# Kernel optimization log

Hardware: AMD Instinct MI355X
Metric: run time of the kernel (lower is better)

The kernel has to match this reference:

```python
import jax, jax.numpy as jnp
import numpy as np


def setup_inputs() -> dict:
    key = jax.random.key(0)
    k1, k2, k3 = jax.random.split(key, 3)
    N, C, Nf, W, H = 8, 256, 16, 28, 28
    l = jax.random.normal(k1, (N, C, Nf, W, H), dtype=jnp.float32)
    g = jax.random.normal(k2, (N, C, 1, 1, 1), dtype=jnp.float32)
    # 1x1x1 Conv3d(in=C, out=1, bias=False) weight collapses to a length-C vector
    w = jax.random.normal(k3, (C,), dtype=jnp.float32) * (1.0 / np.sqrt(C))
    return {"l": l, "g": g, "w": w}


def reference(l, g, w):
    # l: [N,C,Nf,W,H], g broadcastable to l, w: [C]
    N, C, Nf, W, H = l.shape
    # compatibility score: channel dot-product (1x1x1 conv, out_channels=1)
    c = jnp.einsum('ncfwh,c->nfwh', l + g, w)                      # [N,Nf,W,H]
    # softmax over the spatial dims (W*H) per frame, normalize_attn=True
    a = jax.nn.softmax(c.reshape(N, Nf, W * H), axis=-1)           # [N,Nf,WH]
    a = a.reshape(N, Nf, W, H)
    # attention-weighted spatial sum pooling -> [N,C,Nf]
    g_out = jnp.einsum('nfwh,ncfwh->ncf', a, l)
    # module returns raw compatibility map (pre-softmax) squeezed, and pooled g
    return (c, g_out)
```

## Files before the change

kernel.cpp:

```cpp
#include <hip/hip_runtime.h>
#include <math.h>

constexpr int N_ = 8, C_ = 256, F_ = 16, WH_ = 784;
constexpr int CH_STRIDE = F_ * WH_;
constexpr int COUT_SZ = N_ * F_ * WH_;

__device__ inline float wave_reduce_sum(float v) {
#pragma unroll
  for (int o = 32; o > 0; o >>= 1) v += __shfl_down(v, o, 64);
  return v;
}
__device__ inline float wave_reduce_max(float v) {
#pragma unroll
  for (int o = 32; o > 0; o >>= 1) v = fmaxf(v, __shfl_down(v, o, 64));
  return v;
}

__global__ __launch_bounds__(1024) void mfla_kernel(
    const float* __restrict__ l, const float* __restrict__ g,
    const float* __restrict__ w, float* __restrict__ out) {
  __shared__ float w_s[C_];
  __shared__ float e_s[WH_];
  __shared__ float red_s[16];
  __shared__ float bc_s;

  const int b = blockIdx.x;
  const int n = b >> 4;
  const int f = b & 15;
  const int tid = threadIdx.x;
  const int lane = tid & 63;
  const int wv = tid >> 6;

  if (tid < C_) w_s[tid] = w[tid];

  float gv = (tid < C_) ? g[n * C_ + tid] * w[tid] : 0.f;
  gv = wave_reduce_sum(gv);
  if (lane == 0) red_s[wv] = gv;
  __syncthreads();
  if (tid == 0) {
    float s = 0.f;
#pragma unroll
    for (int i = 0; i < 16; ++i) s += red_s[i];
    bc_s = s;
  }
  __syncthreads();
  const float gb = bc_s;

  const size_t base_nf = (size_t)(n * C_ * F_ + f) * WH_;
  float cv = -3.4e38f;
  if (tid < WH_) {
    const float* lp = l + base_nf + tid;
    float acc = 0.f;
#pragma unroll 8
    for (int c = 0; c < C_; ++c) acc = fmaf(lp[(size_t)c * CH_STRIDE], w_s[c], acc);
    cv = acc + gb;
    out[b * WH_ + tid] = cv;
  }

  float m = wave_reduce_max(cv);
  __syncthreads();
  if (lane == 0) red_s[wv] = m;
  __syncthreads();
  if (tid == 0) {
    float mm = red_s[0];
#pragma unroll
    for (int i = 1; i < 16; ++i) mm = fmaxf(mm, red_s[i]);
    bc_s = mm;
  }
  __syncthreads();
  const float cmax = bc_s;

  float e = 0.f;
  if (tid < WH_) {
    e = expf(cv - cmax);
    e_s[tid] = e;
  }
  float s = wave_reduce_sum(e);
  __syncthreads();
  if (lane == 0) red_s[wv] = s;
  __syncthreads();
  if (tid == 0) {
    float ss = 0.f;
#pragma unroll
    for (int i = 0; i < 16; ++i) ss += red_s[i];
    bc_s = 1.f / ss;
  }
  __syncthreads();
  const float inv_sum = bc_s;

  const int p0 = lane << 2;
  const float4 ew0 = *reinterpret_cast<const float4*>(&e_s[p0]);
  const float4 ew1 = *reinterpret_cast<const float4*>(&e_s[p0 + 256]);
  const float4 ew2 = *reinterpret_cast<const float4*>(&e_s[p0 + 512]);
  float4 ew3 = make_float4(0.f, 0.f, 0.f, 0.f);
  if (lane < 4) ew3 = *reinterpret_cast<const float4*>(&e_s[768 + p0]);

#pragma unroll 1
  for (int i = 0; i < 16; ++i) {
    const int c = wv + (i << 4);
    const float* bp = l + ((size_t)(n * C_ + c) * F_ + f) * WH_;
    float4 lv0 = *reinterpret_cast<const float4*>(bp + p0);
    float4 lv1 = *reinterpret_cast<const float4*>(bp + p0 + 256);
    float4 lv2 = *reinterpret_cast<const float4*>(bp + p0 + 512);
    float4 lv3 = make_float4(0.f, 0.f, 0.f, 0.f);
    if (lane < 4) lv3 = *reinterpret_cast<const float4*>(bp + 768 + p0);

    float acc = 0.f;
    acc = fmaf(lv0.x, ew0.x, acc); acc = fmaf(lv0.y, ew0.y, acc);
    acc = fmaf(lv0.z, ew0.z, acc); acc = fmaf(lv0.w, ew0.w, acc);
    acc = fmaf(lv1.x, ew1.x, acc); acc = fmaf(lv1.y, ew1.y, acc);
    acc = fmaf(lv1.z, ew1.z, acc); acc = fmaf(lv1.w, ew1.w, acc);
    acc = fmaf(lv2.x, ew2.x, acc); acc = fmaf(lv2.y, ew2.y, acc);
    acc = fmaf(lv2.z, ew2.z, acc); acc = fmaf(lv2.w, ew2.w, acc);
    acc = fmaf(lv3.x, ew3.x, acc); acc = fmaf(lv3.y, ew3.y, acc);
    acc = fmaf(lv3.z, ew3.z, acc); acc = fmaf(lv3.w, ew3.w, acc);

    acc = wave_reduce_sum(acc);
    if (lane == 0)
      out[COUT_SZ + (size_t)(n * C_ + c) * F_ + f] = acc * inv_sum;
  }
}

extern "C" void kernel_launch(void* const* d_in, const int* in_sizes, int n_in,
                              void* d_out, int out_size, void* d_ws, size_t ws_size,
                              hipStream_t stream) {
  const float* l = (const float*)d_in[0];
  const float* g = (const float*)d_in[1];
  const float* w = (const float*)d_in[2];
  float* out = (float*)d_out;
  mfla_kernel<<<dim3(N_ * F_), dim3(1024), 0, stream>>>(l, g, w, out);
}
```

Baseline: 166.9 us.

## Split fused attention kernel into three kernels with channel-split partial sums

Replaces the single 128-block fused kernel with three launches. The first computes channel-split partial dot products across 2048 blocks. The second reduces the partials, adds the g term and computes the softmax into a workspace. The third pools l against the normalized attention with one block per (n, c) and contiguous float4 reads. The aim is to fill the GPU with far more blocks than the original 128, at the cost of reading l twice, extra workspace traffic and three launch overheads.

```diff
diff --git a/kernel.cpp b/kernel.cpp
--- a/kernel.cpp
+++ b/kernel.cpp
@@ -2,8 +2,12 @@
 #include <math.h>
 
 constexpr int N_ = 8, C_ = 256, F_ = 16, WH_ = 784;
+constexpr int NF = N_ * F_;
 constexpr int CH_STRIDE = F_ * WH_;
-constexpr int COUT_SZ = N_ * F_ * WH_;
+constexpr int SPLITS = 16;
+constexpr int CPS = C_ / SPLITS;
+constexpr int COUT_SZ = NF * WH_;
+constexpr int P4 = WH_ / 4;
 
 __device__ inline float wave_reduce_sum(float v) {
 #pragma unroll
@@ -16,108 +20,125 @@
   return v;
 }
 
-__global__ __launch_bounds__(1024) void mfla_kernel(
-    const float* __restrict__ l, const float* __restrict__ g,
-    const float* __restrict__ w, float* __restrict__ out) {
-  __shared__ float w_s[C_];
-  __shared__ float e_s[WH_];
-  __shared__ float red_s[16];
-  __shared__ float bc_s;
+__global__ __launch_bounds__(256) void k1_partial(
+    const float* __restrict__ l, const float* __restrict__ w,
+    float* __restrict__ part) {
+  const int b = blockIdx.x;
+  const int nf = b >> 4;
+  const int s = b & 15;
+  const int n = nf >> 4, f = nf & 15;
+  const int t = threadIdx.x;
+  if (t >= P4) return;
 
-  const int b = blockIdx.x;
-  const int n = b >> 4;
-  const int f = b & 15;
-  const int tid = threadIdx.x;
-  const int lane = tid & 63;
-  const int wv = tid >> 6;
+  const float* base = l + ((size_t)(n * C_ + s * CPS) * F_ + f) * WH_ + 4 * t;
+  const float* wp = w + s * CPS;
+  float4 acc = make_float4(0.f, 0.f, 0.f, 0.f);
+#pragma unroll
+  for (int j = 0; j < CPS; ++j) {
+    const float wj = wp[j];
+    const float4 v = *reinterpret_cast<const float4*>(base + (size_t)j * CH_STRIDE);
+    acc.x = fmaf(v.x, wj, acc.x);
+    acc.y = fmaf(v.y, wj, acc.y);
+    acc.z = fmaf(v.z, wj, acc.z);
+    acc.w = fmaf(v.w, wj, acc.w);
+  }
+  *reinterpret_cast<float4*>(part + (size_t)b * WH_ + 4 * t) = acc;
+}
 
-  if (tid < C_) w_s[tid] = w[tid];
+__global__ __launch_bounds__(256) void k2_softmax(
+    const float* __restrict__ part, const float* __restrict__ g,
+    const float* __restrict__ w, float* __restrict__ out,
+    float* __restrict__ a) {
+  __shared__ float red[4];
+  __shared__ float bc;
+  const int nf = blockIdx.x;
+  const int n = nf >> 4;
+  const int t = threadIdx.x;
+  const int lane = t & 63, wv = t >> 6;
 
-  float gv = (tid < C_) ? g[n * C_ + tid] * w[tid] : 0.f;
+  float gv = g[n * C_ + t] * w[t];
   gv = wave_reduce_sum(gv);
-  if (lane == 0) red_s[wv] = gv;
+  if (lane == 0) red[wv] = gv;
   __syncthreads();
-  if (tid == 0) {
-    float s = 0.f;
+  if (t == 0) bc = red[0] + red[1] + red[2] + red[3];
+  __syncthreads();
+  const float gb = bc;
+
+  float4 cv = make_float4(-3.4e38f, -3.4e38f, -3.4e38f, -3.4e38f);
+  if (t < P4) {
+    const float* pp = part + (size_t)nf * SPLITS * WH_ + 4 * t;
+    float4 s0 = make_float4(0.f, 0.f, 0.f, 0.f);
 #pragma unroll
-    for (int i = 0; i < 16; ++i) s += red_s[i];
-    bc_s = s;
-  }
-  __syncthreads();
-  const float gb = bc_s;
-
-  const size_t base_nf = (size_t)(n * C_ * F_ + f) * WH_;
-  float cv = -3.4e38f;
-  if (tid < WH_) {
-    const float* lp = l + base_nf + tid;
-    float acc = 0.f;
-#pragma unroll 8
-    for (int c = 0; c < C_; ++c) acc = fmaf(lp[(size_t)c * CH_STRIDE], w_s[c], acc);
-    cv = acc + gb;
-    out[b * WH_ + tid] = cv;
+    for (int s = 0; s < SPLITS; ++s) {
+      const float4 v = *reinterpret_cast<const float4*>(pp + (size_t)s * WH_);
+      s0.x += v.x; s0.y += v.y; s0.z += v.z; s0.w += v.w;
+    }
+    cv = make_float4(s0.x + gb, s0.y + gb, s0.z + gb, s0.w + gb);
+    *reinterpret_cast<float4*>(out + (size_t)nf * WH_ + 4 * t) = cv;
   }
 
-  float m = wave_reduce_max(cv);
+  float m = fmaxf(fmaxf(cv.x, cv.y), fmaxf(cv.z, cv.w));
+  m = wave_reduce_max(m);
   __syncthreads();
-  if (lane == 0) red_s[wv] = m;
+  if (lane == 0) red[wv] = m;
   __syncthreads();
-  if (tid == 0) {
-    float mm = red_s[0];
+  if (t == 0) bc = fmaxf(fmaxf(red[0], red[1]), fmaxf(red[2], red[3]));
+  __syncthreads();
+  const float cmax = bc;
+
+  float4 e = make_float4(0.f, 0.f, 0.f, 0.f);
+  if (t < P4) {
+    e.x = expf(cv.x - cmax);
+    e.y = expf(cv.y - cmax);
+    e.z = expf(cv.z - cmax);
+    e.w = expf(cv.w - cmax);
+  }
+  float ssum = (e.x + e.y) + (e.z + e.w);
+  ssum = wave_reduce_sum(ssum);
+  __syncthreads();
+  if (lane == 0) red[wv] = ssum;
+  __syncthreads();
+  if (t == 0) bc = 1.f / (red[0] + red[1] + red[2] + red[3]);
+  __syncthreads();
+  const float inv = bc;
+
+  if (t < P4) {
+    e.x *= inv; e.y *= inv; e.z *= inv; e.w *= inv;
+    *reinterpret_cast<float4*>(a + (size_t)nf * WH_ + 4 * t) = e;
+  }
+}
+
+__global__ __launch_bounds__(256) void k3_pool(
+    const float* __restrict__ l, const float* __restrict__ a,
+    float* __restrict__ out) {
+  const int b = blockIdx.x;
+  const int n = b >> 8;
+  const int t = threadIdx.x, lane = t & 63, wv = t >> 6;
+  const float* lb = l + (size_t)b * CH_STRIDE;
+  const float* ab = a + (size_t)n * F_ * WH_;
+
 #pragma unroll
-    for (int i = 1; i < 16; ++i) mm = fmaxf(mm, red_s[i]);
-    bc_s = mm;
-  }
-  __syncthreads();
-  const float cmax = bc_s;
-
-  float e = 0.f;
-  if (tid < WH_) {
-    e = expf(cv - cmax);
-    e_s[tid] = e;
-  }
-  float s = wave_reduce_sum(e);
-  __syncthreads();
-  if (lane == 0) red_s[wv] = s;
-  __syncthreads();
-  if (tid == 0) {
-    float ss = 0.f;
-#pragma unroll
-    for (int i = 0; i < 16; ++i) ss += red_s[i];
-    bc_s = 1.f / ss;
-  }
-  __syncthreads();
-  const float inv_sum = bc_s;
-
-  const int p0 = lane << 2;
-  const float4 ew0 = *reinterpret_cast<const float4*>(&e_s[p0]);
-  const float4 ew1 = *reinterpret_cast<const float4*>(&e_s[p0 + 256]);
-  const float4 ew2 = *reinterpret_cast<const float4*>(&e_s[p0 + 512]);
-  float4 ew3 = make_float4(0.f, 0.f, 0.f, 0.f);
-  if (lane < 4) ew3 = *reinterpret_cast<const float4*>(&e_s[768 + p0]);
-
-#pragma unroll 1
-  for (int i = 0; i < 16; ++i) {
-    const int c = wv + (i << 4);
-    const float* bp = l + ((size_t)(n * C_ + c) * F_ + f) * WH_;
-    float4 lv0 = *reinterpret_cast<const float4*>(bp + p0);
-    float4 lv1 = *reinterpret_cast<const float4*>(bp + p0 + 256);
-    float4 lv2 = *reinterpret_cast<const float4*>(bp + p0 + 512);
-    float4 lv3 = make_float4(0.f, 0.f, 0.f, 0.f);
-    if (lane < 4) lv3 = *reinterpret_cast<const float4*>(bp + 768 + p0);
-
+  for (int i = 0; i < 4; ++i) {
+    const int f = wv * 4 + i;
+    const float4* lf = reinterpret_cast<const float4*>(lb + f * WH_);
+    const float4* af = reinterpret_cast<const float4*>(ab + f * WH_);
+    const float4 x0 = lf[lane],       y0 = af[lane];
+    const float4 x1 = lf[lane + 64],  y1 = af[lane + 64];
+    const float4 x2 = lf[lane + 128], y2 = af[lane + 128];
     float acc = 0.f;
-    acc = fmaf(lv0.x, ew0.x, acc); acc = fmaf(lv0.y, ew0.y, acc);
-    acc = fmaf(lv0.z, ew0.z, acc); acc = fmaf(lv0.w, ew0.w, acc);
-    acc = fmaf(lv1.x, ew1.x, acc); acc = fmaf(lv1.y, ew1.y, acc);
-    acc = fmaf(lv1.z, ew1.z, acc); acc = fmaf(lv1.w, ew1.w, acc);
-    acc = fmaf(lv2.x, ew2.x, acc); acc = fmaf(lv2.y, ew2.y, acc);
-    acc = fmaf(lv2.z, ew2.z, acc); acc = fmaf(lv2.w, ew2.w, acc);
-    acc = fmaf(lv3.x, ew3.x, acc); acc = fmaf(lv3.y, ew3.y, acc);
-    acc = fmaf(lv3.z, ew3.z, acc); acc = fmaf(lv3.w, ew3.w, acc);
-
+    acc = fmaf(x0.x, y0.x, acc); acc = fmaf(x0.y, y0.y, acc);
+    acc = fmaf(x0.z, y0.z, acc); acc = fmaf(x0.w, y0.w, acc);
+    acc = fmaf(x1.x, y1.x, acc); acc = fmaf(x1.y, y1.y, acc);
+    acc = fmaf(x1.z, y1.z, acc); acc = fmaf(x1.w, y1.w, acc);
+    acc = fmaf(x2.x, y2.x, acc); acc = fmaf(x2.y, y2.y, acc);
+    acc = fmaf(x2.z, y2.z, acc); acc = fmaf(x2.w, y2.w, acc);
+    if (lane < 4) {
+      const float4 x3 = lf[lane + 192], y3 = af[lane + 192];
+      acc = fmaf(x3.x, y3.x, acc); acc = fmaf(x3.y, y3.y, acc);
+      acc = fmaf(x3.z, y3.z, acc); acc = fmaf(x3.w, y3.w, acc);
+    }
     acc = wave_reduce_sum(acc);
-    if (lane == 0)
-      out[COUT_SZ + (size_t)(n * C_ + c) * F_ + f] = acc * inv_sum;
+    if (lane == 0) out[COUT_SZ + (size_t)b * F_ + f] = acc;
   }
 }
 
@@ -128,5 +149,10 @@
   const float* g = (const float*)d_in[1];
   const float* w = (const float*)d_in[2];
   float* out = (float*)d_out;
-  mfla_kernel<<<dim3(N_ * F_), dim3(1024), 0, stream>>>(l, g, w, out);
+  float* part = (float*)d_ws;
+  float* a = part + (size_t)SPLITS * NF * WH_;
+
+  k1_partial<<<dim3(NF * SPLITS), dim3(256), 0, stream>>>(l, w, part);
+  k2_softmax<<<dim3(NF), dim3(256), 0, stream>>>(part, g, w, out, a);
+  k3_pool<<<dim3(N_ * C_), dim3(256), 0, stream>>>(l, a, out);
 }
```

Measured after the change: 170.4 us. 1.02x slower.
